# Optimization experiments

Measured on AMD Instinct MI355X. Metric: run time of the kernel, lower is better.

## Reference

```python
import jax, jax.numpy as jnp
import numpy as np

N_NODES = 100000
N_EDGES = 1600000
IN, HID, OUT = 32, 32, 16


def setup_inputs() -> dict:
    key = jax.random.key(0)
    ks = jax.random.split(key, 8)
    return {
        "features": jax.random.normal(ks[0], (N_NODES, IN), dtype=jnp.float32),
        "src": jax.random.randint(ks[1], (N_EDGES,), 0, N_NODES, dtype=jnp.int32),
        "dst": jax.random.randint(ks[2], (N_EDGES,), 0, N_NODES, dtype=jnp.int32),
        "edge_weight": jax.random.uniform(ks[3], (N_EDGES,), dtype=jnp.float32),
        "W1": jax.random.normal(ks[4], (IN, HID), dtype=jnp.float32) * 0.1,
        "b1": jnp.zeros((HID,), dtype=jnp.float32),
        "W2": jax.random.normal(ks[5], (HID, OUT), dtype=jnp.float32) * 0.1,
        "b2": jnp.zeros((OUT,), dtype=jnp.float32),
    }


def _graph_conv(h, W, b, src, dst, edge_weight, norm_src, norm_dst, n):
    # DGL GraphConv, norm='both', with edge_weight (u_mul_e aggregation)
    h = h * norm_src[:, None]          # out-degree^-0.5 on source side
    h = h @ W                          # dense transform (tiny GEMM)
    m = h[src] * edge_weight[:, None]  # gather + edge weighting  [E, d]
    agg = jax.ops.segment_sum(m, dst, num_segments=n)  # scatter-add SpMM
    return agg * norm_dst[:, None] + b # in-degree^-0.5 + bias


def reference(features, src, dst, edge_weight, W1, b1, W2, b2):
    n = features.shape[0]
    ones_e = jnp.ones_like(edge_weight)
    deg_out = jnp.clip(jax.ops.segment_sum(ones_e, src, num_segments=n), 1.0)
    deg_in = jnp.clip(jax.ops.segment_sum(ones_e, dst, num_segments=n), 1.0)
    norm_src = deg_out ** -0.5
    norm_dst = deg_in ** -0.5
    h = _graph_conv(features, W1, b1, src, dst, edge_weight, norm_src, norm_dst, n)
    h = jax.nn.relu(h)
    # dropout is identity in eval mode
    h = _graph_conv(h, W2, b2, src, dst, edge_weight, norm_src, norm_dst, n)
    return h
```

## Files before the change

### kernel.cpp

```cpp
#include <hip/hip_runtime.h>
#include <hip/hip_fp16.h>


#define NB   391
#define CAPB 5504
#define EPB  4096

__device__ __forceinline__ long nt_load_i64(const long* p) {
    return __builtin_nontemporal_load(p);
}

__global__ __launch_bounds__(256) void partition_kernel(
        const int* __restrict__ src, const int* __restrict__ dst,
        const float* __restrict__ ew,
        int* __restrict__ g_cur_d, int* __restrict__ g_cur_s,
        int2* __restrict__ pack_part, unsigned char* __restrict__ src_part, int m) {
    __shared__ int hist_d[NB], hist_s[NB];
    __shared__ int lbase_d[NB], lbase_s[NB];
    __shared__ int gbase_d[NB], gbase_s[NB];
    __shared__ int cur_d[NB], cur_s[NB];
    __shared__ int sc[2][512];
    __shared__ long stage[EPB];
    __shared__ unsigned short dbuck[EPB];
    __shared__ unsigned char  sstage[EPB];
    __shared__ unsigned short sbuck[EPB];
    int t = threadIdx.x;
    for (int i = t; i < NB; i += 256) {
        hist_d[i] = 0; hist_s[i] = 0; cur_d[i] = 0; cur_s[i] = 0;
    }
    __syncthreads();
    int base_e = blockIdx.x * EPB;
    int total = m - base_e; if (total > EPB) total = EPB;
    int es[16], ed[16]; float wv[16];
#pragma unroll
    for (int k = 0; k < 16; k++) {
        int e = base_e + k * 256 + t;
        if (e < m) { es[k] = src[e]; ed[k] = dst[e]; wv[k] = ew[e]; }
        else ed[k] = -1;
    }
#pragma unroll
    for (int k = 0; k < 16; k++) {
        if (ed[k] >= 0) {
            atomicAdd(&hist_d[ed[k] >> 8], 1);
            atomicAdd(&hist_s[es[k] >> 8], 1);
        }
    }
    __syncthreads();
    for (int i = t; i < 512; i += 256) sc[0][i] = (i < NB) ? hist_d[i] : 0;
    __syncthreads();
    int pp = 0;
    for (int off = 1; off < 512; off <<= 1) {
        for (int i = t; i < 512; i += 256)
            sc[1 - pp][i] = sc[pp][i] + (i >= off ? sc[pp][i - off] : 0);
        __syncthreads();
        pp ^= 1;
    }
    for (int i = t; i < NB; i += 256) lbase_d[i] = sc[pp][i] - hist_d[i];
    __syncthreads();
    for (int i = t; i < 512; i += 256) sc[0][i] = (i < NB) ? hist_s[i] : 0;
    __syncthreads();
    pp = 0;
    for (int off = 1; off < 512; off <<= 1) {
        for (int i = t; i < 512; i += 256)
            sc[1 - pp][i] = sc[pp][i] + (i >= off ? sc[pp][i - off] : 0);
        __syncthreads();
        pp ^= 1;
    }
    for (int i = t; i < NB; i += 256) lbase_s[i] = sc[pp][i] - hist_s[i];
    __syncthreads();
    for (int i = t; i < NB; i += 256) {
        int c = hist_d[i];
        gbase_d[i] = i * CAPB + (c ? atomicAdd(&g_cur_d[i], c) : 0);
        c = hist_s[i];
        gbase_s[i] = i * CAPB + (c ? atomicAdd(&g_cur_s[i], c) : 0);
    }
    __syncthreads();
#pragma unroll
    for (int k = 0; k < 16; k++) {
        if (ed[k] >= 0) {
            int d = ed[k], s = es[k];
            int bd = d >> 8;
            int r = atomicAdd(&cur_d[bd], 1);
            int pos = lbase_d[bd] + r;
            stage[pos] = (long)(unsigned int)(s | ((d & 255) << 20)) |
                         ((long)__float_as_int(wv[k]) << 32);
            dbuck[pos] = (unsigned short)bd;
            int bs = s >> 8;
            int rs = atomicAdd(&cur_s[bs], 1);
            int ps = lbase_s[bs] + rs;
            sstage[ps] = (unsigned char)(s & 255);
            sbuck[ps] = (unsigned short)bs;
        }
    }
    __syncthreads();
    long* packl = (long*)pack_part;
    for (int i = t; i < total; i += 256) {
        int b = dbuck[i];
        packl[(size_t)gbase_d[b] + (i - lbase_d[b])] = stage[i];
    }
    for (int i = t; i < total; i += 256) {
        int b = sbuck[i];
        src_part[(size_t)gbase_s[b] + (i - lbase_s[b])] = sstage[i];
    }
}

__global__ void csr_kernel(const int2* __restrict__ pack_part,
                           const unsigned char* __restrict__ src_part,
                           const int* __restrict__ g_cur_d, const int* __restrict__ g_cur_s,
                           int2* __restrict__ csr, int2* __restrict__ rs_cnt,
                           float* __restrict__ norm_src, float* __restrict__ norm_dst, int n) {
    __shared__ int cnt[256];
    __shared__ int rowx[256];
    __shared__ int cur[256];
    __shared__ int cnt_s[256];
    extern __shared__ int2 stage[];
    int t = threadIdx.x, b = blockIdx.x;
    if (t < 256) { cnt[t] = 0; cur[t] = 0; cnt_s[t] = 0; }
    __syncthreads();
    int count = g_cur_d[b]; if (count > CAPB) count = CAPB;
    int count_s = g_cur_s[b]; if (count_s > CAPB) count_s = CAPB;
    const int2* p = pack_part + (size_t)b * CAPB;
    const unsigned char* sp = src_part + (size_t)b * CAPB;
    for (int e = t; e < count; e += 512) atomicAdd(&cnt[p[e].x >> 20], 1);
    for (int e = t; e < count_s; e += 512) atomicAdd(&cnt_s[sp[e]], 1);
    __syncthreads();
    if (t < 256) {
        int node = b * 256 + t;
        if (node < n) {
            int cs = cnt_s[t];
            norm_src[node] = rsqrtf((float)(cs > 1 ? cs : 1));
        }
    }
    int c0 = 0;
    if (t < 256) { c0 = cnt[t]; rowx[t] = c0; }
    __syncthreads();
    for (int off = 1; off < 256; off <<= 1) {
        int v = 0;
        if (t < 256 && t >= off) v = rowx[t - off];
        __syncthreads();
        if (t < 256) rowx[t] += v;
        __syncthreads();
    }
    if (t < 256) {
        int excl = rowx[t] - c0;
        rowx[t] = excl;
        int node = b * 256 + t;
        if (node < n) {
            rs_cnt[node] = make_int2(b * CAPB + excl, c0);
            norm_dst[node] = rsqrtf((float)(c0 > 1 ? c0 : 1));
        }
    }
    __syncthreads();
    for (int e = t; e < count; e += 512) {
        int2 v = p[e];
        int dl = v.x >> 20;
        int r = atomicAdd(&cur[dl], 1);
        stage[rowx[dl] + r] = make_int2(v.x & 0x1FFFF, v.y);
    }
    __syncthreads();
    int2* outp = csr + (size_t)b * CAPB;
    for (int e = t; e < count; e += 512) outp[e] = stage[e];
}

__global__ void transform1_kernel(const float* __restrict__ feat,
                                  const float* __restrict__ norm_src,
                                  const float* __restrict__ W1,
                                  __half* __restrict__ h1, int n) {
    __shared__ float sW[32 * 32];
    __shared__ float sF[8][32];
    int t = threadIdx.x;
    for (int i = t; i < 32 * 32; i += 256) sW[i] = W1[i];
    int node0 = blockIdx.x * 8;
    int local = t >> 5, col = t & 31;
    int node = node0 + local;
    float f = 0.0f;
    if (node < n) f = feat[node * 32 + col] * norm_src[node];
    sF[local][col] = f;
    __syncthreads();
    if (node < n) {
        float acc = 0.0f;
#pragma unroll
        for (int k = 0; k < 32; k++) acc += sF[local][k] * sW[k * 32 + col];
        h1[(size_t)node * 32 + col] = __float2half(acc);
    }
}

__global__ void gather1_fused_kernel(const __half* __restrict__ h1, const int2* __restrict__ csr,
                                     const int2* __restrict__ rs_cnt,
                                     const float* __restrict__ norm_src, const float* __restrict__ norm_dst,
                                     const float* __restrict__ W2, const float* __restrict__ b1,
                                     __half* __restrict__ h2, int n) {
    __shared__ float sW2[32 * 16];
    __shared__ float sX[4][4][32];
    int t = threadIdx.x;
    for (int i = t; i < 512; i += 256) sW2[i] = W2[i];
    __syncthreads();
    int w = t >> 6, lane = t & 63;
    int q = lane >> 4;
    int dh = lane & 15;
    int node = (blockIdx.x * 4 + w) * 4 + q;
    bool valid = node < n;
    int2 rc = valid ? rs_cnt[node] : make_int2(0, 0);
    long base = rc.x;
    int c = rc.y;
    const __half2* tv = (const __half2*)h1;
    const long* csrl = (const long*)csr;
    float ax0 = 0.f, ay0 = 0.f, ax1 = 0.f, ay1 = 0.f;
    float ax2 = 0.f, ay2 = 0.f, ax3 = 0.f, ay3 = 0.f;
    int j = 0;
    for (; j + 3 < c; j += 4) {
        long q0 = nt_load_i64(csrl + base + j);
        long q1 = nt_load_i64(csrl + base + j + 1);
        long q2 = nt_load_i64(csrl + base + j + 2);
        long q3 = nt_load_i64(csrl + base + j + 3);
        float2 v0 = __half22float2(tv[(size_t)(int)q0 * 16 + dh]);
        float2 v1 = __half22float2(tv[(size_t)(int)q1 * 16 + dh]);
        float2 v2 = __half22float2(tv[(size_t)(int)q2 * 16 + dh]);
        float2 v3 = __half22float2(tv[(size_t)(int)q3 * 16 + dh]);
        float w0 = __int_as_float((int)(q0 >> 32)), w1 = __int_as_float((int)(q1 >> 32));
        float w2 = __int_as_float((int)(q2 >> 32)), w3 = __int_as_float((int)(q3 >> 32));
        ax0 += v0.x * w0; ay0 += v0.y * w0;
        ax1 += v1.x * w1; ay1 += v1.y * w1;
        ax2 += v2.x * w2; ay2 += v2.y * w2;
        ax3 += v3.x * w3; ay3 += v3.y * w3;
    }
    for (; j < c; j++) {
        long qq = nt_load_i64(csrl + base + j);
        float2 v = __half22float2(tv[(size_t)(int)qq * 16 + dh]);
        float ww = __int_as_float((int)(qq >> 32));
        ax0 += v.x * ww; ay0 += v.y * ww;
    }
    float ax = (ax0 + ax1) + (ax2 + ax3);
    float ay = (ay0 + ay1) + (ay2 + ay3);
    if (valid) {
        float nd = norm_dst[node], ns = norm_src[node];
        sX[w][q][2 * dh]     = fmaxf(ax * nd + b1[2 * dh],     0.0f) * ns;
        sX[w][q][2 * dh + 1] = fmaxf(ay * nd + b1[2 * dh + 1], 0.0f) * ns;
    }
    if (valid) {
        float o = 0.0f;
#pragma unroll
        for (int k = 0; k < 32; k++) o += sX[w][q][k] * sW2[k * 16 + dh];
        h2[(size_t)node * 16 + dh] = __float2half(o);
    }
}

__global__ void gather2_kernel(const __half* __restrict__ h2, const int2* __restrict__ csr,
                               const int2* __restrict__ rs_cnt,
                               const float* __restrict__ norm_dst, const float* __restrict__ b2,
                               float* __restrict__ out, int n) {
    int t = threadIdx.x;
    int w = t >> 6, lane = t & 63;
    int q = lane >> 3;
    int dh = lane & 7;
    int node = (blockIdx.x * 4 + w) * 8 + q;
    bool valid = node < n;
    int2 rc = valid ? rs_cnt[node] : make_int2(0, 0);
    long base = rc.x;
    int c = rc.y;
    const __half2* tv = (const __half2*)h2;
    const long* csrl = (const long*)csr;
    float ax0 = 0.f, ay0 = 0.f, ax1 = 0.f, ay1 = 0.f;
    float ax2 = 0.f, ay2 = 0.f, ax3 = 0.f, ay3 = 0.f;
    int j = 0;
    for (; j + 3 < c; j += 4) {
        long q0 = nt_load_i64(csrl + base + j);
        long q1 = nt_load_i64(csrl + base + j + 1);
        long q2 = nt_load_i64(csrl + base + j + 2);
        long q3 = nt_load_i64(csrl + base + j + 3);
        float2 v0 = __half22float2(tv[(size_t)(int)q0 * 8 + dh]);
        float2 v1 = __half22float2(tv[(size_t)(int)q1 * 8 + dh]);
        float2 v2 = __half22float2(tv[(size_t)(int)q2 * 8 + dh]);
        float2 v3 = __half22float2(tv[(size_t)(int)q3 * 8 + dh]);
        float w0 = __int_as_float((int)(q0 >> 32)), w1 = __int_as_float((int)(q1 >> 32));
        float w2 = __int_as_float((int)(q2 >> 32)), w3 = __int_as_float((int)(q3 >> 32));
        ax0 += v0.x * w0; ay0 += v0.y * w0;
        ax1 += v1.x * w1; ay1 += v1.y * w1;
        ax2 += v2.x * w2; ay2 += v2.y * w2;
        ax3 += v3.x * w3; ay3 += v3.y * w3;
    }
    for (; j < c; j++) {
        long qq = nt_load_i64(csrl + base + j);
        float2 v = __half22float2(tv[(size_t)(int)qq * 8 + dh]);
        float ww = __int_as_float((int)(qq >> 32));
        ax0 += v.x * ww; ay0 += v.y * ww;
    }
    float ax = (ax0 + ax1) + (ax2 + ax3);
    float ay = (ay0 + ay1) + (ay2 + ay3);
    if (valid) {
        float nd = norm_dst[node];
        float2 o;
        o.x = ax * nd + b2[2 * dh];
        o.y = ay * nd + b2[2 * dh + 1];
        ((float2*)out)[(size_t)node * 8 + dh] = o;
    }
}

extern "C" void kernel_launch(void* const* d_in, const int* in_sizes, int n_in,
                              void* d_out, int out_size, void* d_ws, size_t ws_size,
                              hipStream_t stream) {
    const float* feat = (const float*)d_in[0];
    const int*   src  = (const int*)d_in[1];
    const int*   dst  = (const int*)d_in[2];
    const float* ew   = (const float*)d_in[3];
    const float* W1   = (const float*)d_in[4];
    const float* b1   = (const float*)d_in[5];
    const float* W2   = (const float*)d_in[6];
    const float* b2   = (const float*)d_in[7];
    float* out = (float*)d_out;

    const int n = in_sizes[0] / 32;
    const int m = in_sizes[1];

    char* wsb = (char*)d_ws;
    int2*   pack_part = (int2*)wsb;
    int2*   csr       = pack_part + (size_t)NB * CAPB;
    __half* h1        = (__half*)(csr + (size_t)NB * CAPB);
    __half* h2        = h1 + 32 * (size_t)n;
    float*  norm_src  = (float*)(h2 + 16 * (size_t)n);
    float*  norm_dst  = norm_src + n;
    int2*   rs_cnt    = (int2*)(norm_dst + n);
    int*    g_cur_d   = (int*)(rs_cnt + n);
    int*    g_cur_s   = g_cur_d + NB;
    unsigned char* src_part = (unsigned char*)(g_cur_s + NB);

    hipMemsetAsync(g_cur_d, 0, 2 * NB * sizeof(int), stream);

    partition_kernel<<<(m + EPB - 1) / EPB, 256, 0, stream>>>(src, dst, ew, g_cur_d, g_cur_s,
                                                              pack_part, src_part, m);
    csr_kernel<<<NB, 512, CAPB * sizeof(int2), stream>>>(pack_part, src_part, g_cur_d, g_cur_s,
                                                         csr, rs_cnt, norm_src, norm_dst, n);
    transform1_kernel<<<(n + 7) / 8, 256, 0, stream>>>(feat, norm_src, W1, h1, n);
    gather1_fused_kernel<<<(n + 15) / 16, 256, 0, stream>>>(h1, csr, rs_cnt,
                                                            norm_src, norm_dst, W2, b1, h2, n);
    gather2_kernel<<<(n + 31) / 32, 256, 0, stream>>>(h2, csr, rs_cnt, norm_dst, b2, out, n);
}
```

Measured before the change: 208.9 us.

## Fuse layer-1 dense transform into CSR kernel and halve partition block size

The separate transform1 kernel is removed. Its feature scaling and 32x32 matmul now run at the end of csr_kernel, reusing the staging shared memory and the per-node norm_src values the block has just computed. This saves one kernel launch and the global reload of norm_src. Separately, the partition kernel now handles 2048 edges per block instead of 4096, which gives more blocks and less register and shared-memory use per block, but also more global atomics and smaller contiguous writes per bucket. The fused transform runs on only 391 blocks, so it may have less parallelism than the old launch.

```diff
diff --git a/kernel.cpp b/kernel.cpp
--- a/kernel.cpp
+++ b/kernel.cpp
@@ -4,7 +4,7 @@
 
 #define NB   391
 #define CAPB 5504
-#define EPB  4096
+#define EPB  2048
 
 __device__ __forceinline__ long nt_load_i64(const long* p) {
     return __builtin_nontemporal_load(p);
@@ -31,15 +31,15 @@
     __syncthreads();
     int base_e = blockIdx.x * EPB;
     int total = m - base_e; if (total > EPB) total = EPB;
-    int es[16], ed[16]; float wv[16];
-#pragma unroll
-    for (int k = 0; k < 16; k++) {
+    int es[8], ed[8]; float wv[8];
+#pragma unroll
+    for (int k = 0; k < 8; k++) {
         int e = base_e + k * 256 + t;
         if (e < m) { es[k] = src[e]; ed[k] = dst[e]; wv[k] = ew[e]; }
         else ed[k] = -1;
     }
 #pragma unroll
-    for (int k = 0; k < 16; k++) {
+    for (int k = 0; k < 8; k++) {
         if (ed[k] >= 0) {
             atomicAdd(&hist_d[ed[k] >> 8], 1);
             atomicAdd(&hist_s[es[k] >> 8], 1);
@@ -76,7 +76,7 @@
     }
     __syncthreads();
 #pragma unroll
-    for (int k = 0; k < 16; k++) {
+    for (int k = 0; k < 8; k++) {
         if (ed[k] >= 0) {
             int d = ed[k], s = es[k];
             int bd = d >> 8;
@@ -107,15 +107,20 @@
 __global__ void csr_kernel(const int2* __restrict__ pack_part,
                            const unsigned char* __restrict__ src_part,
                            const int* __restrict__ g_cur_d, const int* __restrict__ g_cur_s,
+                           const float* __restrict__ feat, const float* __restrict__ W1,
                            int2* __restrict__ csr, int2* __restrict__ rs_cnt,
-                           float* __restrict__ norm_src, float* __restrict__ norm_dst, int n) {
+                           float* __restrict__ norm_src, float* __restrict__ norm_dst,
+                           __half* __restrict__ h1, int n) {
     __shared__ int cnt[256];
     __shared__ int rowx[256];
     __shared__ int cur[256];
     __shared__ int cnt_s[256];
+    __shared__ float nsrc[256];
+    __shared__ float sW1[1024];
     extern __shared__ int2 stage[];
     int t = threadIdx.x, b = blockIdx.x;
     if (t < 256) { cnt[t] = 0; cur[t] = 0; cnt_s[t] = 0; }
+    for (int i = t; i < 1024; i += 512) sW1[i] = W1[i];
     __syncthreads();
     int count = g_cur_d[b]; if (count > CAPB) count = CAPB;
     int count_s = g_cur_s[b]; if (count_s > CAPB) count_s = CAPB;
@@ -128,8 +133,10 @@
         int node = b * 256 + t;
         if (node < n) {
             int cs = cnt_s[t];
-            norm_src[node] = rsqrtf((float)(cs > 1 ? cs : 1));
-        }
+            float ns = rsqrtf((float)(cs > 1 ? cs : 1));
+            nsrc[t] = ns;
+            norm_src[node] = ns;
+        } else nsrc[t] = 0.0f;
     }
     int c0 = 0;
     if (t < 256) { c0 = cnt[t]; rowx[t] = c0; }
@@ -160,28 +167,21 @@
     __syncthreads();
     int2* outp = csr + (size_t)b * CAPB;
     for (int e = t; e < count; e += 512) outp[e] = stage[e];
-}
-
-__global__ void transform1_kernel(const float* __restrict__ feat,
-                                  const float* __restrict__ norm_src,
-                                  const float* __restrict__ W1,
-                                  __half* __restrict__ h1, int n) {
-    __shared__ float sW[32 * 32];
-    __shared__ float sF[8][32];
-    int t = threadIdx.x;
-    for (int i = t; i < 32 * 32; i += 256) sW[i] = W1[i];
-    int node0 = blockIdx.x * 8;
-    int local = t >> 5, col = t & 31;
-    int node = node0 + local;
-    float f = 0.0f;
-    if (node < n) f = feat[node * 32 + col] * norm_src[node];
-    sF[local][col] = f;
-    __syncthreads();
-    if (node < n) {
+    __syncthreads();
+    float* sF = (float*)stage;
+    int node0 = b * 256;
+    int lim = n - node0; if (lim > 256) lim = 256; if (lim < 0) lim = 0;
+    for (int o = t; o < lim * 32; o += 512) {
+        int i = o >> 5, k = o & 31;
+        sF[o] = feat[(size_t)(node0 + i) * 32 + k] * nsrc[i];
+    }
+    __syncthreads();
+    for (int o = t; o < lim * 32; o += 512) {
+        int i = o >> 5, col = o & 31;
         float acc = 0.0f;
 #pragma unroll
-        for (int k = 0; k < 32; k++) acc += sF[local][k] * sW[k * 32 + col];
-        h1[(size_t)node * 32 + col] = __float2half(acc);
+        for (int k = 0; k < 32; k++) acc += sF[i * 32 + k] * sW1[k * 32 + col];
+        h1[(size_t)(node0 + i) * 32 + col] = __float2half(acc);
     }
 }
 
@@ -329,8 +329,8 @@
     partition_kernel<<<(m + EPB - 1) / EPB, 256, 0, stream>>>(src, dst, ew, g_cur_d, g_cur_s,
                                                               pack_part, src_part, m);
     csr_kernel<<<NB, 512, CAPB * sizeof(int2), stream>>>(pack_part, src_part, g_cur_d, g_cur_s,
-                                                         csr, rs_cnt, norm_src, norm_dst, n);
-    transform1_kernel<<<(n + 7) / 8, 256, 0, stream>>>(feat, norm_src, W1, h1, n);
+                                                         feat, W1, csr, rs_cnt,
+                                                         norm_src, norm_dst, h1, n);
     gather1_fused_kernel<<<(n + 15) / 16, 256, 0, stream>>>(h1, csr, rs_cnt,
                                                             norm_src, norm_dst, W2, b1, h2, n);
     gather2_kernel<<<(n + 31) / 32, 256, 0, stream>>>(h2, csr, rs_cnt, norm_dst, b2, out, n);
```

Result: slower. 230.1 us (+10.2%).
